# Performance work log

Hardware: AMD Instinct MI355X
Metric: run time of the kernel (lower is better)

Reference implementation:

```python
import jax, jax.numpy as jnp
import numpy as np

B, S, D, H = 4, 2048, 1024, 16
HD = D // H  # head_dim = 64


def setup_inputs() -> dict:
    key = jax.random.key(0)
    ks = jax.random.split(key, 11)
    scale = 1.0 / np.sqrt(D)
    q = jax.random.normal(ks[0], (B, S, D), jnp.float32)
    k = jax.random.normal(ks[1], (B, S, D), jnp.float32)
    v = jax.random.normal(ks[2], (B, S, D), jnp.float32)
    # causal mask, broadcastable over [B, H, Sq, Sk]
    mask = jnp.tril(jnp.ones((S, S), bool))[None, None, :, :]
    Wq = jax.random.normal(ks[3], (D, D), jnp.float32) * scale
    bq = jnp.zeros((D,), jnp.float32)
    Wk = jax.random.normal(ks[4], (D, D), jnp.float32) * scale
    bk = jnp.zeros((D,), jnp.float32)
    Wv = jax.random.normal(ks[5], (D, D), jnp.float32) * scale
    bv = jnp.zeros((D,), jnp.float32)
    Wo = jax.random.normal(ks[6], (D, D), jnp.float32) * scale
    bo = jnp.zeros((D,), jnp.float32)
    return {"q": q, "k": k, "v": v, "mask": mask,
            "Wq": Wq, "bq": bq, "Wk": Wk, "bk": bk,
            "Wv": Wv, "bv": bv, "Wo": Wo, "bo": bo}


def reference(q, k, v, mask, Wq, bq, Wk, bk, Wv, bv, Wo, bo):
    b, sq, _ = q.shape
    sk = k.shape[1]
    # projections (torch Linear: x @ W.T + b)
    qh = (q @ Wq.T + bq).reshape(b, sq, H, HD)
    kh = (k @ Wk.T + bk).reshape(b, sk, H, HD)
    vh = (v @ Wv.T + bv).reshape(b, sk, H, HD)
    # scaled dot-product attention: [b, h, sq, sk]
    scores = jnp.einsum('bqhd,bkhd->bhqk', qh, kh) / jnp.sqrt(jnp.float32(HD))
    scores = jnp.where(mask, scores, jnp.float32(-jnp.inf))
    attn = jax.nn.softmax(scores, axis=-1)
    out = jnp.einsum('bhqk,bkhd->bqhd', attn, vh).reshape(b, sq, D)
    return out @ Wo.T + bo
```

## Files before the change

kernel.cpp:

```cpp
#include <hip/hip_runtime.h>
#include <hip/hip_bf16.h>
#include <cstdint>
#include <cstddef>

typedef __attribute__((ext_vector_type(4))) float f32x4;
typedef __attribute__((ext_vector_type(8))) __bf16 bf16x8;

constexpr int Bc = 4, Sc = 2048, Dc = 1024, Hc = 16, HDc = 64;
constexpr int Mrows = Bc * Sc;
constexpr int Kdim = Dc;
constexpr int Ndim = Dc;

__device__ __forceinline__ void gload_lds16(const void* g, void* lds) {
  __builtin_amdgcn_global_load_lds(
      (const __attribute__((address_space(1))) void*)g,
      (__attribute__((address_space(3))) void*)lds, 16, 0, 0);
}

__global__ void cvt_f32_to_bf16(const float* __restrict__ src,
                                __bf16* __restrict__ dst, int n4) {
  int i = blockIdx.x * blockDim.x + threadIdx.x;
  if (i >= n4) return;
  float4 f = ((const float4*)src)[i];
  union { __bf16 h[4]; uint2 u; } p;
  p.h[0] = (__bf16)f.x; p.h[1] = (__bf16)f.y;
  p.h[2] = (__bf16)f.z; p.h[3] = (__bf16)f.w;
  ((uint2*)dst)[i] = p.u;
}

template<int OUT_MODE>
__global__ __launch_bounds__(256, 2)
void gemm_bt(const __bf16* __restrict__ A, const __bf16* __restrict__ Bw,
             const float* __restrict__ bias, void* __restrict__ outp,
             float scale)
{
  __shared__ __align__(16) __bf16 As[128 * 32];
  __shared__ __align__(16) __bf16 Bs[128 * 32];
  const int tid = threadIdx.x;
  const int wave = tid >> 6, lane = tid & 63;
  const int wr = wave >> 1, wc = wave & 1;
  const int r = lane & 15, hi = lane >> 4;
  const int m0 = blockIdx.y * 128, n0 = blockIdx.x * 128;

  f32x4 acc[4][4] = {};

  for (int k0 = 0; k0 < Kdim; k0 += 32) {
    #pragma unroll
    for (int c = 0; c < 2; ++c) {
      int chunk = c * 256 + wave * 64 + lane;
      int row = chunk >> 2;
      int hc = (chunk & 3) ^ (row & 3);
      gload_lds16(A  + (size_t)(m0 + row) * Kdim + k0 + hc * 8,
                  &As[(size_t)(c * 256 + wave * 64) * 8]);
      gload_lds16(Bw + (size_t)(n0 + row) * Kdim + k0 + hc * 8,
                  &Bs[(size_t)(c * 256 + wave * 64) * 8]);
    }
    __syncthreads();
    bf16x8 af[4], bfr[4];
    #pragma unroll
    for (int m = 0; m < 4; ++m) {
      int rowl = wr * 64 + m * 16 + r;
      af[m] = *(const bf16x8*)&As[rowl * 32 + ((hi ^ (rowl & 3)) * 8)];
    }
    #pragma unroll
    for (int n = 0; n < 4; ++n) {
      int rowl = wc * 64 + n * 16 + r;
      bfr[n] = *(const bf16x8*)&Bs[rowl * 32 + ((hi ^ (rowl & 3)) * 8)];
    }
    #pragma unroll
    for (int m = 0; m < 4; ++m)
      #pragma unroll
      for (int n = 0; n < 4; ++n)
        acc[m][n] = __builtin_amdgcn_mfma_f32_16x16x32_bf16(af[m], bfr[n], acc[m][n], 0, 0, 0);
    __syncthreads();
  }

  if (OUT_MODE == 2) {
    #pragma unroll
    for (int m = 0; m < 4; ++m)
      #pragma unroll
      for (int n = 0; n < 4; ++n) {
        int row0 = m0 + wr * 64 + m * 16 + hi * 4;
        int col  = n0 + wc * 64 + n * 16 + r;
        int b = row0 >> 11, s = row0 & (Sc - 1);
        int h = col >> 6, d = col & 63;
        union { __bf16 hh[4]; uint2 u; } w;
        #pragma unroll
        for (int rg = 0; rg < 4; ++rg)
          w.hh[rg] = (__bf16)(acc[m][n][rg] + bias[col]);
        *(uint2*)&((__bf16*)outp)[(((size_t)(b * Hc + h) * HDc + d) << 11) + s] = w.u;
      }
  } else {
    #pragma unroll
    for (int m = 0; m < 4; ++m)
      #pragma unroll
      for (int n = 0; n < 4; ++n)
        #pragma unroll
        for (int rg = 0; rg < 4; ++rg) {
          int row_g = m0 + wr * 64 + m * 16 + hi * 4 + rg;
          int col_g = n0 + wc * 64 + n * 16 + r;
          float v = (acc[m][n][rg] + bias[col_g]) * scale;
          if (OUT_MODE == 0) {
            int b = row_g >> 11, s = row_g & (Sc - 1);
            int h = col_g >> 6, d = col_g & 63;
            ((__bf16*)outp)[((((size_t)b * Hc + h) * Sc + s) << 6) + d] = (__bf16)v;
          } else {
            ((float*)outp)[(size_t)row_g * Dc + col_g] = v;
          }
        }
  }
}

__global__ __launch_bounds__(128, 2)
void attn_causal(const __bf16* __restrict__ Qh, const __bf16* __restrict__ Kh,
                 const __bf16* __restrict__ Vt, __bf16* __restrict__ outp)
{
  const int tid = threadIdx.x;
  const int wave = tid >> 6, lane = tid & 63;
  const int r = lane & 15, hi = lane >> 4;
  const int bh = blockIdx.y;
  const int qt = wave ? (31 - (int)blockIdx.x) : (int)blockIdx.x;
  const int q0 = qt * 64;
  const __bf16* Q = Qh + (size_t)bh * (Sc * HDc);
  const __bf16* K = Kh + (size_t)bh * (Sc * HDc);
  const __bf16* V = Vt + (size_t)bh * (HDc * Sc);

  bf16x8 qf[4][2];
  #pragma unroll
  for (int m = 0; m < 4; ++m)
    #pragma unroll
    for (int kc = 0; kc < 2; ++kc)
      qf[m][kc] = *(const bf16x8*)&Q[(size_t)(q0 + m * 16 + r) * 64 + kc * 32 + hi * 8];

  f32x4 o_acc[4][4] = {};
  float mrow[4], lrow[4];
  #pragma unroll
  for (int m = 0; m < 4; ++m) { mrow[m] = -1e30f; lrow[m] = 0.f; }

  const int T = qt + 1;
  bf16x8 kf[4][2], vf[4][2], pb[4][2];

  #pragma unroll
  for (int n = 0; n < 4; ++n)
    #pragma unroll
    for (int kc = 0; kc < 2; ++kc) {
      kf[n][kc] = *(const bf16x8*)&K[(size_t)(n * 16 + r) * 64 + kc * 32 + hi * 8];
      vf[n][kc] = *(const bf16x8*)&V[(size_t)(n * 16 + r) * Sc + kc * 32 + hi * 8];
    }

  for (int t = 0; t < T; ++t) {
    const bool diag = (t == T - 1);
    const int kvn = (t + 1) * 64;

    #pragma unroll
    for (int m = 0; m < 4; ++m) {
      f32x4 sn[4];
      #pragma unroll
      for (int n = 0; n < 4; ++n) {
        f32x4 z = {0.f, 0.f, 0.f, 0.f};
        sn[n] = __builtin_amdgcn_mfma_f32_16x16x32_bf16(kf[n][0], qf[m][0], z, 0, 0, 0);
        sn[n] = __builtin_amdgcn_mfma_f32_16x16x32_bf16(kf[n][1], qf[m][1], sn[n], 0, 0, 0);
      }
      if (diag) {
        #pragma unroll
        for (int n = 0; n < 4; ++n)
          #pragma unroll
          for (int rg = 0; rg < 4; ++rg)
            if (n * 16 + hi * 4 + rg > m * 16 + r) sn[n][rg] = -1e30f;
      }
      float mx = fmaxf(fmaxf(fmaxf(sn[0][0], sn[0][1]), fmaxf(sn[0][2], sn[0][3])),
                       fmaxf(fmaxf(sn[1][0], sn[1][1]), fmaxf(sn[1][2], sn[1][3])));
      mx = fmaxf(mx, fmaxf(fmaxf(fmaxf(sn[2][0], sn[2][1]), fmaxf(sn[2][2], sn[2][3])),
                           fmaxf(fmaxf(sn[3][0], sn[3][1]), fmaxf(sn[3][2], sn[3][3]))));
      mx = fmaxf(mx, __shfl_xor(mx, 16));
      mx = fmaxf(mx, __shfl_xor(mx, 32));
      float mnew = fmaxf(mrow[m], mx);
      float sc = __expf(mrow[m] - mnew);
      mrow[m] = mnew;
      float rs = 0.f;
      #pragma unroll
      for (int n = 0; n < 4; ++n)
        #pragma unroll
        for (int rg = 0; rg < 4; ++rg) {
          float p = __expf(sn[n][rg] - mnew);
          sn[n][rg] = p;
          rs += p;
        }
      rs += __shfl_xor(rs, 16);
      rs += __shfl_xor(rs, 32);
      lrow[m] = lrow[m] * sc + rs;
      #pragma unroll
      for (int n = 0; n < 4; ++n) o_acc[m][n] *= sc;

      #pragma unroll
      for (int kc = 0; kc < 2; ++kc) {
        uint32_t p0a, p0b, p1a, p1b;
        asm("v_cvt_pk_bf16_f32 %0, %1, %2" : "=v"(p0a) : "v"(sn[2*kc][0]),   "v"(sn[2*kc][1]));
        asm("v_cvt_pk_bf16_f32 %0, %1, %2" : "=v"(p0b) : "v"(sn[2*kc][2]),   "v"(sn[2*kc][3]));
        asm("v_cvt_pk_bf16_f32 %0, %1, %2" : "=v"(p1a) : "v"(sn[2*kc+1][0]), "v"(sn[2*kc+1][1]));
        asm("v_cvt_pk_bf16_f32 %0, %1, %2" : "=v"(p1b) : "v"(sn[2*kc+1][2]), "v"(sn[2*kc+1][3]));
        asm("v_permlane32_swap_b32 %0, %1" : "+v"(p0a), "+v"(p1a));
        asm("v_permlane32_swap_b32 %0, %1" : "+v"(p0b), "+v"(p1b));
        uint32_t Xa = (uint32_t)__shfl_xor((int)p1a, 16);
        uint32_t Xb = (uint32_t)__shfl_xor((int)p1b, 16);
        uint32_t Ya = (uint32_t)__shfl_xor((int)p0a, 16);
        uint32_t Yb = (uint32_t)__shfl_xor((int)p0b, 16);
        union { uint32_t u[4]; bf16x8 v; } pk;
        pk.u[0] = (hi & 1) ? Xa : p0a;
        pk.u[1] = (hi & 1) ? Xb : p0b;
        pk.u[2] = (hi & 1) ? p1a : Ya;
        pk.u[3] = (hi & 1) ? p1b : Yb;
        pb[m][kc] = pk.v;
      }
    }

    if (t + 1 < T) {
      #pragma unroll
      for (int n = 0; n < 4; ++n)
        #pragma unroll
        for (int kc = 0; kc < 2; ++kc)
          kf[n][kc] = *(const bf16x8*)&K[(size_t)(kvn + n * 16 + r) * 64 + kc * 32 + hi * 8];
    }

    #pragma unroll
    for (int m = 0; m < 4; ++m)
      #pragma unroll
      for (int n = 0; n < 4; ++n) {
        o_acc[m][n] = __builtin_amdgcn_mfma_f32_16x16x32_bf16(vf[n][0], pb[m][0], o_acc[m][n], 0, 0, 0);
        o_acc[m][n] = __builtin_amdgcn_mfma_f32_16x16x32_bf16(vf[n][1], pb[m][1], o_acc[m][n], 0, 0, 0);
      }

    if (t + 1 < T) {
      #pragma unroll
      for (int n = 0; n < 4; ++n)
        #pragma unroll
        for (int kc = 0; kc < 2; ++kc)
          vf[n][kc] = *(const bf16x8*)&V[(size_t)(n * 16 + r) * Sc + kvn + kc * 32 + hi * 8];
    }
  }

  const int b = bh >> 4, h = bh & 15;
  #pragma unroll
  for (int m = 0; m < 4; ++m) {
    float inv = 1.f / lrow[m];
    size_t row = (size_t)b * Sc + q0 + m * 16 + r;
    #pragma unroll
    for (int n = 0; n < 4; ++n) {
      union { __bf16 hh[4]; uint2 u; } w;
      #pragma unroll
      for (int rg = 0; rg < 4; ++rg)
        w.hh[rg] = (__bf16)(o_acc[m][n][rg] * inv);
      int col = h * 64 + n * 16 + hi * 4;
      *(uint2*)&outp[row * Dc + col] = w.u;
    }
  }
}

extern "C" void kernel_launch(void* const* d_in, const int* in_sizes, int n_in,
                              void* d_out, int out_size, void* d_ws, size_t ws_size,
                              hipStream_t stream) {
  const float* q  = (const float*)d_in[0];
  const float* k  = (const float*)d_in[1];
  const float* v  = (const float*)d_in[2];
  const float* Wq = (const float*)d_in[4];
  const float* bq = (const float*)d_in[5];
  const float* Wk = (const float*)d_in[6];
  const float* bk = (const float*)d_in[7];
  const float* Wv = (const float*)d_in[8];
  const float* bv = (const float*)d_in[9];
  const float* Wo = (const float*)d_in[10];
  const float* bo = (const float*)d_in[11];

  char* ws = (char*)d_ws;
  constexpr size_t MB = 1u << 20;
  __bf16* Wqb = (__bf16*)(ws + 0 * MB);
  __bf16* Wkb = (__bf16*)(ws + 2 * MB);
  __bf16* Wvb = (__bf16*)(ws + 4 * MB);
  __bf16* Wob = (__bf16*)(ws + 6 * MB);
  __bf16* Xbf = (__bf16*)(ws + 8 * MB);
  __bf16* QhB = (__bf16*)(ws + 24 * MB);
  __bf16* KhB = (__bf16*)(ws + 40 * MB);
  __bf16* VtB = (__bf16*)(ws + 56 * MB);

  const int nW4 = (Dc * Dc) / 4;
  const int nX4 = (Mrows * Dc) / 4;
  cvt_f32_to_bf16<<<(nW4 + 255) / 256, 256, 0, stream>>>(Wq, Wqb, nW4);
  cvt_f32_to_bf16<<<(nW4 + 255) / 256, 256, 0, stream>>>(Wk, Wkb, nW4);
  cvt_f32_to_bf16<<<(nW4 + 255) / 256, 256, 0, stream>>>(Wv, Wvb, nW4);
  cvt_f32_to_bf16<<<(nW4 + 255) / 256, 256, 0, stream>>>(Wo, Wob, nW4);

  dim3 gg(Ndim / 128, Mrows / 128);
  cvt_f32_to_bf16<<<(nX4 + 255) / 256, 256, 0, stream>>>(q, Xbf, nX4);
  gemm_bt<0><<<gg, 256, 0, stream>>>(Xbf, Wqb, bq, QhB, 0.125f);
  cvt_f32_to_bf16<<<(nX4 + 255) / 256, 256, 0, stream>>>(k, Xbf, nX4);
  gemm_bt<0><<<gg, 256, 0, stream>>>(Xbf, Wkb, bk, KhB, 1.0f);
  cvt_f32_to_bf16<<<(nX4 + 255) / 256, 256, 0, stream>>>(v, Xbf, nX4);
  gemm_bt<2><<<gg, 256, 0, stream>>>(Xbf, Wvb, bv, VtB, 1.0f);

  attn_causal<<<dim3(16, Bc * Hc), 128, 0, stream>>>(QhB, KhB, VtB, Xbf);

  gemm_bt<1><<<gg, 256, 0, stream>>>(Xbf, Wob, bo, d_out, 1.0f);
}
```

Baseline: 285.4 us.

## Split KV range across two waves per query tile with LDS merge, lazy rescale, exp2

The attention kernel now gives each block a single query tile and splits its KV tiles between two waves. The partial softmax states are merged through shared memory at the end, which doubles the grid and evens out causal imbalance. It also folds log2(e) into the Q scale so it can use exp2, and only rescales the running max when it grows by more than a threshold. It also raises MFMA wave priority and lifts occupancy bounds. The four weight conversions are fused into one launch. The merge adds LDS traffic and a barrier, and the lazy rescale bounds exponent growth to 2^8.

```diff
diff --git a/kernel.cpp b/kernel.cpp
--- a/kernel.cpp
+++ b/kernel.cpp
@@ -26,6 +26,21 @@
   p.h[0] = (__bf16)f.x; p.h[1] = (__bf16)f.y;
   p.h[2] = (__bf16)f.z; p.h[3] = (__bf16)f.w;
   ((uint2*)dst)[i] = p.u;
+}
+
+__global__ void cvt4_f32_to_bf16(const float* __restrict__ s0, const float* __restrict__ s1,
+                                 const float* __restrict__ s2, const float* __restrict__ s3,
+                                 __bf16* __restrict__ d0, __bf16* __restrict__ d1,
+                                 __bf16* __restrict__ d2, __bf16* __restrict__ d3, int n4each) {
+  int i = blockIdx.x * blockDim.x + threadIdx.x;
+  int which = i / n4each, j = i - which * n4each;
+  const float* s = which == 0 ? s0 : which == 1 ? s1 : which == 2 ? s2 : s3;
+  __bf16* d = which == 0 ? d0 : which == 1 ? d1 : which == 2 ? d2 : d3;
+  float4 f = ((const float4*)s)[j];
+  union { __bf16 h[4]; uint2 u; } p;
+  p.h[0] = (__bf16)f.x; p.h[1] = (__bf16)f.y;
+  p.h[2] = (__bf16)f.z; p.h[3] = (__bf16)f.w;
+  ((uint2*)d)[j] = p.u;
 }
 
 template<int OUT_MODE>
@@ -111,15 +126,19 @@
   }
 }
 
-__global__ __launch_bounds__(128, 2)
+__global__ __launch_bounds__(128, 4)
 void attn_causal(const __bf16* __restrict__ Qh, const __bf16* __restrict__ Kh,
                  const __bf16* __restrict__ Vt, __bf16* __restrict__ outp)
 {
+  __shared__ __align__(16) float OaS[4][4][64][4];
+  __shared__ float MS[4][64];
+  __shared__ float LS[4][64];
+
   const int tid = threadIdx.x;
   const int wave = tid >> 6, lane = tid & 63;
   const int r = lane & 15, hi = lane >> 4;
   const int bh = blockIdx.y;
-  const int qt = wave ? (31 - (int)blockIdx.x) : (int)blockIdx.x;
+  const int qt = 31 - (int)blockIdx.x;
   const int q0 = qt * 64;
   const __bf16* Q = Qh + (size_t)bh * (Sc * HDc);
   const __bf16* K = Kh + (size_t)bh * (Sc * HDc);
@@ -138,29 +157,35 @@
   for (int m = 0; m < 4; ++m) { mrow[m] = -1e30f; lrow[m] = 0.f; }
 
   const int T = qt + 1;
+  const int half = (T + 1) >> 1;
+  const int t0 = wave ? half : 0;
+  const int t1 = wave ? T : half;
+
   bf16x8 kf[4][2], vf[4][2], pb[4][2];
 
   #pragma unroll
   for (int n = 0; n < 4; ++n)
     #pragma unroll
     for (int kc = 0; kc < 2; ++kc) {
-      kf[n][kc] = *(const bf16x8*)&K[(size_t)(n * 16 + r) * 64 + kc * 32 + hi * 8];
-      vf[n][kc] = *(const bf16x8*)&V[(size_t)(n * 16 + r) * Sc + kc * 32 + hi * 8];
-    }
-
-  for (int t = 0; t < T; ++t) {
+      kf[n][kc] = *(const bf16x8*)&K[(size_t)(t0 * 64 + n * 16 + r) * 64 + kc * 32 + hi * 8];
+      vf[n][kc] = *(const bf16x8*)&V[(size_t)(n * 16 + r) * Sc + t0 * 64 + kc * 32 + hi * 8];
+    }
+
+  for (int t = t0; t < t1; ++t) {
     const bool diag = (t == T - 1);
     const int kvn = (t + 1) * 64;
 
     #pragma unroll
     for (int m = 0; m < 4; ++m) {
       f32x4 sn[4];
+      __builtin_amdgcn_s_setprio(1);
       #pragma unroll
       for (int n = 0; n < 4; ++n) {
         f32x4 z = {0.f, 0.f, 0.f, 0.f};
         sn[n] = __builtin_amdgcn_mfma_f32_16x16x32_bf16(kf[n][0], qf[m][0], z, 0, 0, 0);
         sn[n] = __builtin_amdgcn_mfma_f32_16x16x32_bf16(kf[n][1], qf[m][1], sn[n], 0, 0, 0);
       }
+      __builtin_amdgcn_s_setprio(0);
       if (diag) {
         #pragma unroll
         for (int n = 0; n < 4; ++n)
@@ -174,23 +199,27 @@
                            fmaxf(fmaxf(sn[3][0], sn[3][1]), fmaxf(sn[3][2], sn[3][3]))));
       mx = fmaxf(mx, __shfl_xor(mx, 16));
       mx = fmaxf(mx, __shfl_xor(mx, 32));
-      float mnew = fmaxf(mrow[m], mx);
-      float sc = __expf(mrow[m] - mnew);
-      mrow[m] = mnew;
+      float mloc = mrow[m];
+      if (__any(mx > mloc + 8.f)) {
+        float mnew = fmaxf(mloc, mx);
+        float sc = __builtin_exp2f(mloc - mnew);
+        lrow[m] *= sc;
+        #pragma unroll
+        for (int n = 0; n < 4; ++n) o_acc[m][n] *= sc;
+        mrow[m] = mnew; mloc = mnew;
+      }
       float rs = 0.f;
       #pragma unroll
       for (int n = 0; n < 4; ++n)
         #pragma unroll
         for (int rg = 0; rg < 4; ++rg) {
-          float p = __expf(sn[n][rg] - mnew);
+          float p = __builtin_exp2f(sn[n][rg] - mloc);
           sn[n][rg] = p;
           rs += p;
         }
       rs += __shfl_xor(rs, 16);
       rs += __shfl_xor(rs, 32);
-      lrow[m] = lrow[m] * sc + rs;
-      #pragma unroll
-      for (int n = 0; n < 4; ++n) o_acc[m][n] *= sc;
+      lrow[m] += rs;
 
       #pragma unroll
       for (int kc = 0; kc < 2; ++kc) {
@@ -214,7 +243,7 @@
       }
     }
 
-    if (t + 1 < T) {
+    if (t + 1 < t1) {
       #pragma unroll
       for (int n = 0; n < 4; ++n)
         #pragma unroll
@@ -222,6 +251,7 @@
           kf[n][kc] = *(const bf16x8*)&K[(size_t)(kvn + n * 16 + r) * 64 + kc * 32 + hi * 8];
     }
 
+    __builtin_amdgcn_s_setprio(1);
     #pragma unroll
     for (int m = 0; m < 4; ++m)
       #pragma unroll
@@ -229,8 +259,9 @@
         o_acc[m][n] = __builtin_amdgcn_mfma_f32_16x16x32_bf16(vf[n][0], pb[m][0], o_acc[m][n], 0, 0, 0);
         o_acc[m][n] = __builtin_amdgcn_mfma_f32_16x16x32_bf16(vf[n][1], pb[m][1], o_acc[m][n], 0, 0, 0);
       }
-
-    if (t + 1 < T) {
+    __builtin_amdgcn_s_setprio(0);
+
+    if (t + 1 < t1) {
       #pragma unroll
       for (int n = 0; n < 4; ++n)
         #pragma unroll
@@ -239,19 +270,37 @@
     }
   }
 
-  const int b = bh >> 4, h = bh & 15;
-  #pragma unroll
-  for (int m = 0; m < 4; ++m) {
-    float inv = 1.f / lrow[m];
-    size_t row = (size_t)b * Sc + q0 + m * 16 + r;
-    #pragma unroll
-    for (int n = 0; n < 4; ++n) {
-      union { __bf16 hh[4]; uint2 u; } w;
-      #pragma unroll
-      for (int rg = 0; rg < 4; ++rg)
-        w.hh[rg] = (__bf16)(o_acc[m][n][rg] * inv);
-      int col = h * 64 + n * 16 + hi * 4;
-      *(uint2*)&outp[row * Dc + col] = w.u;
+  if (wave == 1) {
+    #pragma unroll
+    for (int m = 0; m < 4; ++m) {
+      MS[m][lane] = mrow[m];
+      LS[m][lane] = lrow[m];
+      #pragma unroll
+      for (int n = 0; n < 4; ++n)
+        *(f32x4*)OaS[m][n][lane] = o_acc[m][n];
+    }
+  }
+  __syncthreads();
+  if (wave == 0) {
+    const int b = bh >> 4, h = bh & 15;
+    #pragma unroll
+    for (int m = 0; m < 4; ++m) {
+      float mB = MS[m][lane], lB = LS[m][lane];
+      float mF = fmaxf(mrow[m], mB);
+      float aA = __builtin_exp2f(mrow[m] - mF);
+      float aB = __builtin_exp2f(mB - mF);
+      float inv = 1.f / (lrow[m] * aA + lB * aB);
+      size_t row = (size_t)b * Sc + q0 + m * 16 + r;
+      #pragma unroll
+      for (int n = 0; n < 4; ++n) {
+        f32x4 oB = *(f32x4*)OaS[m][n][lane];
+        union { __bf16 hh[4]; uint2 u; } w;
+        #pragma unroll
+        for (int rg = 0; rg < 4; ++rg)
+          w.hh[rg] = (__bf16)((o_acc[m][n][rg] * aA + oB[rg] * aB) * inv);
+        int col = h * 64 + n * 16 + hi * 4;
+        *(uint2*)&outp[row * Dc + col] = w.u;
+      }
     }
   }
 }
@@ -284,20 +333,18 @@
 
   const int nW4 = (Dc * Dc) / 4;
   const int nX4 = (Mrows * Dc) / 4;
-  cvt_f32_to_bf16<<<(nW4 + 255) / 256, 256, 0, stream>>>(Wq, Wqb, nW4);
-  cvt_f32_to_bf16<<<(nW4 + 255) / 256, 256, 0, stream>>>(Wk, Wkb, nW4);
-  cvt_f32_to_bf16<<<(nW4 + 255) / 256, 256, 0, stream>>>(Wv, Wvb, nW4);
-  cvt_f32_to_bf16<<<(nW4 + 255) / 256, 256, 0, stream>>>(Wo, Wob, nW4);
-
+  cvt4_f32_to_bf16<<<(4 * nW4) / 256, 256, 0, stream>>>(Wq, Wk, Wv, Wo, Wqb, Wkb, Wvb, Wob, nW4);
+
+  const float qscale = 0.125f * 1.44269504f;
   dim3 gg(Ndim / 128, Mrows / 128);
   cvt_f32_to_bf16<<<(nX4 + 255) / 256, 256, 0, stream>>>(q, Xbf, nX4);
-  gemm_bt<0><<<gg, 256, 0, stream>>>(Xbf, Wqb, bq, QhB, 0.125f);
+  gemm_bt<0><<<gg, 256, 0, stream>>>(Xbf, Wqb, bq, QhB, qscale);
   cvt_f32_to_bf16<<<(nX4 + 255) / 256, 256, 0, stream>>>(k, Xbf, nX4);
   gemm_bt<0><<<gg, 256, 0, stream>>>(Xbf, Wkb, bk, KhB, 1.0f);
   cvt_f32_to_bf16<<<(nX4 + 255) / 256, 256, 0, stream>>>(v, Xbf, nX4);
   gemm_bt<2><<<gg, 256, 0, stream>>>(Xbf, Wvb, bv, VtB, 1.0f);
 
-  attn_causal<<<dim3(16, Bc * Hc), 128, 0, stream>>>(QhB, KhB, VtB, Xbf);
+  attn_causal<<<dim3(32, Bc * Hc), 128, 0, stream>>>(QhB, KhB, VtB, Xbf);
 
   gemm_bt<1><<<gg, 256, 0, stream>>>(Xbf, Wob, bo, d_out, 1.0f);
 }
```

After: 845.5 us. +196.3%, slower.
